# Performance work log

Hardware: AMD Instinct MI355X
Metric: run time of the kernel (lower is better)

The kernel has to match this reference:

```python
import jax, jax.numpy as jnp
import numpy as np

R = 262144  # 512x512 rays
B = 32      # scene boxes
BIG = 1e10
EPS = 1e-4


def setup_inputs() -> dict:
    key = jax.random.key(0)
    k1, k2, k3, k4 = jax.random.split(key, 4)
    # camera-like ray origins (near a single viewpoint) and unit directions
    rays_o = jax.random.normal(k1, (R, 3), dtype=jnp.float32) * 0.1
    rays_d = jax.random.normal(k2, (R, 3), dtype=jnp.float32)
    rays_d = rays_d / jnp.linalg.norm(rays_d, axis=-1, keepdims=True)
    # axis-aligned boxes: [center_xyz, size_xyz]
    centers = jax.random.uniform(k3, (B, 3), dtype=jnp.float32, minval=-5.0, maxval=5.0)
    sizes = jax.random.uniform(k4, (B, 3), dtype=jnp.float32, minval=0.5, maxval=2.5)
    bbox = jnp.concatenate([centers, sizes], axis=1)
    return {"rays_o": rays_o, "rays_d": rays_d, "bbox": bbox}


def reference(rays_o, rays_d, bbox):
    # rays_d[rays_d == 0] = 1e-8
    rays_d = jnp.where(rays_d == 0.0, 1e-8, rays_d)
    ro = rays_o[:, None, :]  # [R,1,3]
    rd = rays_d[:, None, :]  # [R,1,3]
    bbox_min = bbox[:, :3] - bbox[:, 3:] / 2  # [B,3]
    bbox_max = bbox[:, :3] + bbox[:, 3:] / 2  # [B,3]
    # slab test: per-axis entry/exit parameters, [R,B,3]
    t_mins = (bbox_min - ro) / rd
    t_maxs = (bbox_max - ro) / rd
    t_entry = jnp.minimum(t_mins, t_maxs)  # ts.min(-1)
    t_exit = jnp.maximum(t_mins, t_maxs)   # ts.max(-1)
    t_mins_max = t_entry.max(-1)  # [R,B]
    t_maxs_min = t_exit.min(-1)   # [R,B]
    is_intersects = (t_mins_max < t_maxs_min) & (t_maxs_min > 0)
    keep = is_intersects.any(-1)  # [R]
    # candidate hit points at each per-axis entry t: [R,B,3(axis),3(xyz)]
    t_nears = t_entry
    pts = ro[:, :, None, :] + t_nears[..., None] * rd[:, :, None, :]
    valid = ((pts >= (bbox_min[None, :, None, :] - EPS)) &
             (pts <= (bbox_max[None, :, None, :] + EPS))).all(-1)
    valid = valid & (t_nears >= 0)
    t_nears = jnp.where(valid, t_nears, BIG)
    t_near = t_nears.min(-1)  # [R,B]
    # argsort(...)[:, 0] == argmin over boxes
    first_min = jnp.argmin(t_near, axis=-1)  # [R]
    nearest_bbox_idx = jnp.where(keep, first_min, -1).astype(jnp.int64)
    nearest_distance_2d = jnp.where(
        keep, jnp.take_along_axis(t_near, first_min[:, None], axis=1)[:, 0], -1.0)
    return nearest_bbox_idx, nearest_distance_2d
```

## Files before the change

kernel.cpp:

```cpp
#include <hip/hip_runtime.h>


constexpr int BMAX = 32;

__device__ __forceinline__ float div_markstein(float a, float b, float y) {
    float q0 = __fmul_rn(a, y);
    float e  = __fmaf_rn(-b, q0, a);
    return __fmaf_rn(e, y, q0);
}

template<int B>
__global__ __launch_bounds__(256) void ray_aabb_kernel(
    const float* __restrict__ rays_o,
    const float* __restrict__ rays_d,
    const float* __restrict__ bbox,
    float* __restrict__ out_idx,
    float* __restrict__ out_dist,
    int R)
{
    const float BIG = 10000000000.0f;
    const float EPS = 1e-4f;

    __shared__ float4 s_q[B][3];

    int t = threadIdx.x;
    if (t < B) {
        int b = t;
        float lo[3], hi[3], loE[3], hiE[3];
        #pragma unroll
        for (int a = 0; a < 3; ++a) {
            float c = bbox[b * 6 + a];
            float s = bbox[b * 6 + 3 + a];
            float h  = __fmul_rn(s, 0.5f);
            lo[a]  = __fsub_rn(c, h);
            hi[a]  = __fadd_rn(c, h);
            loE[a] = __fsub_rn(lo[a], EPS);
            hiE[a] = __fadd_rn(hi[a], EPS);
        }
        s_q[b][0] = make_float4(lo[0], lo[1], lo[2], hi[0]);
        s_q[b][1] = make_float4(hi[1], hi[2], loE[0], loE[1]);
        s_q[b][2] = make_float4(loE[2], hiE[0], hiE[1], hiE[2]);
    }
    __syncthreads();

    int i = blockIdx.x * blockDim.x + threadIdx.x;
    if (i >= R) return;

    float ro[3], rd[3], y[3];
    #pragma unroll
    for (int a = 0; a < 3; ++a) {
        ro[a] = rays_o[i * 3 + a];
        float d = rays_d[i * 3 + a];
        rd[a] = (d == 0.0f) ? 1e-8f : d;
        y[a]  = __fdiv_rn(1.0f, rd[a]);
    }

    bool  keep  = false;
    float best  = __builtin_inff();
    int   bestb = 0;

    #pragma unroll 8
    for (int b = 0; b < B; ++b) {
        float4 q0 = s_q[b][0];
        float4 q1 = s_q[b][1];
        float4 q2 = s_q[b][2];
        float lo[3]  = {q0.x, q0.y, q0.z};
        float hi[3]  = {q0.w, q1.x, q1.y};
        float loE[3] = {q1.z, q1.w, q2.x};
        float hiE[3] = {q2.y, q2.z, q2.w};

        float entry[3], exitv[3];
        #pragma unroll
        for (int a = 0; a < 3; ++a) {
            float t1 = div_markstein(__fsub_rn(lo[a], ro[a]), rd[a], y[a]);
            float t2 = div_markstein(__fsub_rn(hi[a], ro[a]), rd[a], y[a]);
            entry[a] = fminf(t1, t2);
            exitv[a] = fmaxf(t1, t2);
        }
        float tmm = fmaxf(entry[0], fmaxf(entry[1], entry[2]));
        float tmx = fminf(exitv[0], fminf(exitv[1], exitv[2]));
        keep = keep || ((tmm < tmx) && (tmx > 0.0f));

        float tn = BIG;
        #pragma unroll
        for (int cnd = 0; cnd < 3; ++cnd) {
            float tc = entry[cnd];
            bool v = (tc >= 0.0f);
            #pragma unroll
            for (int a = 0; a < 3; ++a) {
                if (a == cnd) continue;
                float p = __fadd_rn(ro[a], __fmul_rn(tc, rd[a]));
                v = v && (p >= loE[a]) && (p <= hiE[a]);
            }
            if (v) tn = fminf(tn, tc);
        }
        if (tn < best) { best = tn; bestb = b; }
    }

    out_idx[i]  = keep ? (float)bestb : -1.0f;
    out_dist[i] = keep ? best : -1.0f;
}

extern "C" void kernel_launch(void* const* d_in, const int* in_sizes, int n_in,
                              void* d_out, int out_size, void* d_ws, size_t ws_size,
                              hipStream_t stream) {
    const float* rays_o = (const float*)d_in[0];
    const float* rays_d = (const float*)d_in[1];
    const float* bbox   = (const float*)d_in[2];
    int R = in_sizes[0] / 3;

    float* out = (float*)d_out;
    float* out_idx  = out;
    float* out_dist = out + R;

    const int threads = 256;
    const int blocks = (R + threads - 1) / threads;
    ray_aabb_kernel<BMAX><<<blocks, threads, 0, stream>>>(rays_o, rays_d, bbox,
                                                          out_idx, out_dist, R);
}
```

Measured before the change: 23.83 us.

## Split box loop across two threads per ray and merge via warp shuffle

Each ray is now handled by two adjacent lanes, each testing half of the boxes, and the partial results are combined with xor shuffles before one lane writes the output. The inner box loop is fully unrolled and launch bounds request higher occupancy. This shortens the per-thread serial chain and doubles available parallelism. In exchange, ray loads and reciprocal computation are duplicated, and half the lanes sit idle during the store. Tie-breaking still favours the lower box index.

```diff
diff --git a/kernel.cpp b/kernel.cpp
--- a/kernel.cpp
+++ b/kernel.cpp
@@ -2,6 +2,7 @@
 
 
 constexpr int BMAX = 32;
+constexpr int HALF = BMAX / 2;
 
 __device__ __forceinline__ float div_markstein(float a, float b, float y) {
     float q0 = __fmul_rn(a, y);
@@ -9,8 +10,7 @@
     return __fmaf_rn(e, y, q0);
 }
 
-template<int B>
-__global__ __launch_bounds__(256) void ray_aabb_kernel(
+__global__ __launch_bounds__(256, 8) void ray_aabb_kernel(
     const float* __restrict__ rays_o,
     const float* __restrict__ rays_d,
     const float* __restrict__ bbox,
@@ -21,10 +21,10 @@
     const float BIG = 10000000000.0f;
     const float EPS = 1e-4f;
 
-    __shared__ float4 s_q[B][3];
+    __shared__ float4 s_q[BMAX][3];
 
     int t = threadIdx.x;
-    if (t < B) {
+    if (t < BMAX) {
         int b = t;
         float lo[3], hi[3], loE[3], hiE[3];
         #pragma unroll
@@ -43,24 +43,28 @@
     }
     __syncthreads();
 
-    int i = blockIdx.x * blockDim.x + threadIdx.x;
-    if (i >= R) return;
+    int gid  = blockIdx.x * blockDim.x + threadIdx.x;
+    int ray  = gid >> 1;
+    int par  = gid & 1;
+    if (ray >= R) return;
+    int b0   = par * HALF;
 
     float ro[3], rd[3], y[3];
     #pragma unroll
     for (int a = 0; a < 3; ++a) {
-        ro[a] = rays_o[i * 3 + a];
-        float d = rays_d[i * 3 + a];
+        ro[a] = rays_o[ray * 3 + a];
+        float d = rays_d[ray * 3 + a];
         rd[a] = (d == 0.0f) ? 1e-8f : d;
         y[a]  = __fdiv_rn(1.0f, rd[a]);
     }
 
     bool  keep  = false;
     float best  = __builtin_inff();
-    int   bestb = 0;
+    int   bestb = b0;
 
-    #pragma unroll 8
-    for (int b = 0; b < B; ++b) {
+    #pragma unroll
+    for (int bi = 0; bi < HALF; ++bi) {
+        int b = b0 + bi;
         float4 q0 = s_q[b][0];
         float4 q1 = s_q[b][1];
         float4 q2 = s_q[b][2];
@@ -97,8 +101,17 @@
         if (tn < best) { best = tn; bestb = b; }
     }
 
-    out_idx[i]  = keep ? (float)bestb : -1.0f;
-    out_dist[i] = keep ? best : -1.0f;
+    float o_best  = __shfl_xor(best, 1, 64);
+    int   o_bestb = __shfl_xor(bestb, 1, 64);
+    int   o_keep  = __shfl_xor((int)keep, 1, 64);
+
+    if (par == 0) {
+        bool k = keep || (o_keep != 0);
+        float fb = best; int fi = bestb;
+        if (o_best < fb) { fb = o_best; fi = o_bestb; }
+        out_idx[ray]  = k ? (float)fi : -1.0f;
+        out_dist[ray] = k ? fb : -1.0f;
+    }
 }
 
 extern "C" void kernel_launch(void* const* d_in, const int* in_sizes, int n_in,
@@ -114,7 +127,8 @@
     float* out_dist = out + R;
 
     const int threads = 256;
-    const int blocks = (R + threads - 1) / threads;
-    ray_aabb_kernel<BMAX><<<blocks, threads, 0, stream>>>(rays_o, rays_d, bbox,
-                                                          out_idx, out_dist, R);
+    const long long total = 2LL * R;
+    const int blocks = (int)((total + threads - 1) / threads);
+    ray_aabb_kernel<<<blocks, threads, 0, stream>>>(rays_o, rays_d, bbox,
+                                                    out_idx, out_dist, R);
 }
```

Measured after the change: 72.31 us. +203.5%, slower.
